# Performance work log

Hardware: AMD Instinct MI355X
Metric: run time of the kernel (lower is better)

The kernel has to match this reference:

```python
import jax, jax.numpy as jnp
import numpy as np

N = 50000      # nodes
E = 600000     # edges (avg degree 12)
IN = 128       # in_feat
HID = IN // 2  # 64
OUT = 128      # out_feat (must equal in_feat, see msg_linear)

# NOTE: the torch source uses nn.LeakyReLU(True): the positional arg is
# negative_slope, so slope == 1.0 (identity). We reproduce that faithfully.
NEG_SLOPE = 1.0

def leaky(v):
    return jnp.where(v >= 0, v, NEG_SLOPE * v)

def _linear_params(key, fan_in, fan_out):
    kw, kb = jax.random.split(key)
    bound = 1.0 / np.sqrt(fan_in)
    W = jax.random.uniform(kw, (fan_in, fan_out), jnp.float32, -bound, bound)
    b = jax.random.uniform(kb, (fan_out,), jnp.float32, -bound, bound)
    return W, b

def setup_inputs() -> dict:
    key = jax.random.key(0)
    ks = jax.random.split(key, 10)
    x = jax.random.normal(ks[0], (N, IN), jnp.float32)
    e = jax.random.normal(ks[1], (E, IN), jnp.float32)
    src = jax.random.randint(ks[2], (E,), 0, N, jnp.int64)
    dst = jax.random.randint(ks[3], (E,), 0, N, jnp.int64)
    W_nl1, b_nl1 = _linear_params(ks[4], IN, HID)    # node_linear1
    W_el, b_el = _linear_params(ks[5], IN, HID)      # edge_linear
    W1, b1 = _linear_params(ks[6], HID, HID)         # node_mlp layer 1
    W2, b2 = _linear_params(ks[7], HID, OUT)         # node_mlp layer 2
    W_nl2, b_nl2 = _linear_params(ks[8], IN, HID)    # node_linear2
    km, ke = jax.random.split(ks[9])
    W_ml, b_ml = _linear_params(km, IN, HID)         # msg_linear (in_feat==out_feat)
    W_em, b_em = _linear_params(ke, HID, OUT)        # edge_mlp layer
    return dict(x=x, e=e, src=src, dst=dst,
                W_nl1=W_nl1, b_nl1=b_nl1, W_el=W_el, b_el=b_el,
                W1=W1, b1=b1, W2=W2, b2=b2,
                W_nl2=W_nl2, b_nl2=b_nl2, W_ml=W_ml, b_ml=b_ml,
                W_em=W_em, b_em=b_em)

def reference(x, e, src, dst,
              W_nl1, b_nl1, W_el, b_el,
              W1, b1, W2, b2,
              W_nl2, b_nl2, W_ml, b_ml,
              W_em, b_em):
    # apply_edges: e' = node_mlp(node_linear1(x[src]) + edge_linear(e))
    z = x[src] @ W_nl1 + b_nl1 + e @ W_el + b_el            # [E, HID]
    e_new = leaky(leaky(z) @ W1 + b1) @ W2 + b2             # [E, OUT]
    # update_all(copy_e, sum): scatter-sum edge messages to destination nodes
    msg = jax.ops.segment_sum(e_new, dst, num_segments=N)   # [N, OUT]
    # x' = edge_mlp(node_linear2(x) + msg_linear(msg))
    h = leaky(x @ W_nl2 + b_nl2 + msg @ W_ml + b_ml)        # [N, HID]
    return h @ W_em + b_em                                  # [N, OUT]
```

## Files before the change

kernel.cpp:

```cpp
#include <hip/hip_runtime.h>

#define N_NODES 50000
#define N_EDGES 600000

typedef float v2f __attribute__((ext_vector_type(2)));

#define WF_PX   0
#define WF_ES   3200000
#define WF_PXS  9600000
#define WF_UN   12800000
#define WI_CNT   16000000
#define WI_OFF   16050000
#define WI_CUR   16100000
#define WI_BSUM  16150000
#define WI_BOFF  16150256
#define WI_EPAIR 16150512
#define WF_T2   17350528
#define WF_BEG  17354624
#define WF_RH   17354752
#define WF_K1   17354816
#define WF_WA   17358912
#define WF_WX1  17375296
#define WF_R    17383488
#define WF_C2   17383616

#define NBLK_SCAN 196

__global__ __launch_bounds__(256) void pre_t2_kernel(
        const float* __restrict__ W2, const float* __restrict__ W_ml,
        const float* __restrict__ b1, const float* __restrict__ b2,
        float* __restrict__ T2, float* __restrict__ be_g) {
    int idx = blockIdx.x * 256 + threadIdx.x;
    if (idx < 4096) {
        int i = idx >> 6, j = idx & 63;
        float s = 0.f;
        for (int k = 0; k < 128; ++k) s += W2[i*128+k] * W_ml[k*64+j];
        T2[idx] = s;
    } else if (idx < 4224) {
        int j = idx - 4096;
        float s = b2[j];
        for (int k = 0; k < 64; ++k) s += b1[k] * W2[k*128+j];
        be_g[j] = s;
    }
}

__global__ __launch_bounds__(256) void pre_k1_kernel(
        const float* __restrict__ W1, const float* __restrict__ T2,
        float* __restrict__ K1) {
    int idx = blockIdx.x * 256 + threadIdx.x;
    if (idx >= 4096) return;
    int i = idx >> 6, j = idx & 63;
    float s = 0.f;
    for (int k = 0; k < 64; ++k) s += W1[i*64+k] * T2[k*64+j];
    K1[idx] = s;
}

__global__ __launch_bounds__(256) void pre_wa_kernel(
        const float* __restrict__ W_nl1, const float* __restrict__ W_el,
        const float* __restrict__ W_nl2, const float* __restrict__ K1,
        const float* __restrict__ b_nl1, const float* __restrict__ b_el,
        const float* __restrict__ be_g, const float* __restrict__ W_ml,
        float* __restrict__ WA, float* __restrict__ WX1,
        float* __restrict__ rh_g) {
    int idx = blockIdx.x * 256 + threadIdx.x;
    if (idx < 8192) {
        WA[idx] = W_nl2[idx];
    } else if (idx < 16384) {
        int p = idx - 8192; int i = p >> 6, j = p & 63;
        float s = 0.f;
        for (int k = 0; k < 64; ++k) s += W_el[i*64+k] * K1[k*64+j];
        WA[idx] = s;
    } else if (idx < 24576) {
        int p = idx - 16384; int i = p >> 6, j = p & 63;
        float s = 0.f;
        for (int k = 0; k < 64; ++k) s += W_nl1[i*64+k] * K1[k*64+j];
        WX1[p] = s;
    } else if (idx < 24640) {
        int t = idx - 24576;
        float s = 0.f;
        for (int k = 0; k < 64; ++k)  s += (b_nl1[k] + b_el[k]) * K1[k*64+t];
        for (int k = 0; k < 128; ++k) s += be_g[k] * W_ml[k*64+t];
        rh_g[t] = s;
    }
}

__global__ __launch_bounds__(256) void pre_rc_kernel(
        const float* __restrict__ rh_g, const float* __restrict__ W_em,
        const float* __restrict__ b_nl2, const float* __restrict__ b_ml,
        const float* __restrict__ b_em,
        float* __restrict__ r, float* __restrict__ c2) {
    int idx = threadIdx.x;
    if (idx < 128) {
        float s = 0.f;
        for (int k = 0; k < 64; ++k) s += rh_g[k] * W_em[k*128+idx];
        r[idx] = s;
    } else {
        int j = idx - 128;
        float s = b_em[j];
        for (int k = 0; k < 64; ++k) s += (b_nl2[k] + b_ml[k]) * W_em[k*128+j];
        c2[j] = s;
    }
}

__global__ __launch_bounds__(256) void zero_kernel(int* __restrict__ cnt) {
    int i = blockIdx.x * 256 + threadIdx.x;
    if (i < N_NODES) cnt[i] = 0;
}

__global__ __launch_bounds__(256) void hist_kernel(const int* __restrict__ dst,
                                                   int* __restrict__ cnt) {
    int e = blockIdx.x * 256 + threadIdx.x;
    if (e < N_EDGES) atomicAdd(&cnt[dst[e]], 1);
}

__global__ __launch_bounds__(256) void scan_a_kernel(const int* __restrict__ cnt,
                                                     int* __restrict__ bsum) {
    __shared__ int s[256];
    int i = blockIdx.x * 256 + threadIdx.x;
    int v = (i < N_NODES) ? cnt[i] : 0;
    s[threadIdx.x] = v;
    __syncthreads();
    for (int d = 128; d > 0; d >>= 1) {
        if (threadIdx.x < d) s[threadIdx.x] += s[threadIdx.x + d];
        __syncthreads();
    }
    if (threadIdx.x == 0) bsum[blockIdx.x] = s[0];
}

__global__ __launch_bounds__(256) void scan_b_kernel(const int* __restrict__ bsum,
                                                     int* __restrict__ boff) {
    __shared__ int s[256];
    int t = threadIdx.x;
    int v = (t < NBLK_SCAN) ? bsum[t] : 0;
    s[t] = v;
    __syncthreads();
    for (int d = 1; d < 256; d <<= 1) {
        int tv = (t >= d) ? s[t - d] : 0;
        __syncthreads();
        s[t] += tv;
        __syncthreads();
    }
    if (t < NBLK_SCAN) boff[t] = s[t] - v;
}

__global__ __launch_bounds__(256) void scan_c_kernel(const int* __restrict__ cnt,
                                                     const int* __restrict__ boff,
                                                     int* __restrict__ offs,
                                                     int* __restrict__ cursor) {
    __shared__ int s[256];
    int i = blockIdx.x * 256 + threadIdx.x;
    int t = threadIdx.x;
    int v = (i < N_NODES) ? cnt[i] : 0;
    s[t] = v;
    __syncthreads();
    for (int d = 1; d < 256; d <<= 1) {
        int tv = (t >= d) ? s[t - d] : 0;
        __syncthreads();
        s[t] += tv;
        __syncthreads();
    }
    if (i < N_NODES) {
        int ex = s[t] - v + boff[blockIdx.x];
        offs[i] = ex;
        cursor[i] = ex;
    }
}

__global__ __launch_bounds__(256) void fill_kernel(const int* __restrict__ dst,
                                                   const int* __restrict__ src,
                                                   int* __restrict__ cursor,
                                                   int2* __restrict__ epair) {
    int e = blockIdx.x * 256 + threadIdx.x;
    if (e < N_EDGES) {
        int pos = atomicAdd(&cursor[dst[e]], 1);
        epair[pos] = make_int2(e, src[e]);
    }
}

__global__ __launch_bounds__(256) void px_kernel(
        const float* __restrict__ x, const float* __restrict__ WX1,
        float* __restrict__ px) {
    __shared__ float As[32][133];
    __shared__ float Ws[32][64];
    int base = blockIdx.x * 128;
    int t = threadIdx.x;
    int cg = t & 15, rg = t >> 4;
    int c0 = cg * 4, r0 = rg * 8;

    float acc[8][4];
    #pragma unroll
    for (int i = 0; i < 8; ++i)
        #pragma unroll
        for (int j = 0; j < 4; ++j) acc[i][j] = 0.f;

    int arow0 = t >> 3;
    int akq   = t & 7;

    for (int k0 = 0; k0 < 128; k0 += 32) {
        __syncthreads();
        #pragma unroll
        for (int i = 0; i < 4; ++i) {
            int row = arow0 + i * 32;
            int n = base + row;
            float4 v = make_float4(0.f, 0.f, 0.f, 0.f);
            if (n < N_NODES)
                v = *(const float4*)&x[(size_t)n * 128 + k0 + akq * 4];
            As[akq * 4 + 0][row] = v.x;
            As[akq * 4 + 1][row] = v.y;
            As[akq * 4 + 2][row] = v.z;
            As[akq * 4 + 3][row] = v.w;
        }
        #pragma unroll
        for (int i = 0; i < 2; ++i) {
            int idx = t + i * 256;
            int row = idx >> 4, q4 = idx & 15;
            *(float4*)&Ws[row][q4 * 4] =
                *(const float4*)&WX1[(size_t)(k0 + row) * 64 + q4 * 4];
        }
        __syncthreads();
        #pragma unroll 8
        for (int k = 0; k < 32; ++k) {
            float a[8];
            *(float4*)&a[0] = *(const float4*)&As[k][r0];
            *(float4*)&a[4] = *(const float4*)&As[k][r0 + 4];
            float4 w = *(const float4*)&Ws[k][c0];
            #pragma unroll
            for (int i = 0; i < 8; ++i) {
                acc[i][0] += a[i] * w.x;
                acc[i][1] += a[i] * w.y;
                acc[i][2] += a[i] * w.z;
                acc[i][3] += a[i] * w.w;
            }
        }
    }

    #pragma unroll
    for (int i = 0; i < 8; ++i) {
        int n = base + r0 + i;
        if (n < N_NODES)
            *(float4*)&px[(size_t)n * 64 + c0] = *(float4*)&acc[i][0];
    }
}

__global__ __launch_bounds__(256) void gather_kernel(
        const float* __restrict__ px, const float* __restrict__ ef,
        const int* __restrict__ cnt, const int* __restrict__ offs,
        const int2* __restrict__ epair,
        float* __restrict__ pxs, float* __restrict__ es) {
    int n    = (int)((blockIdx.x * 256 + threadIdx.x) >> 6);
    int lane = threadIdx.x & 63;
    if (n >= N_NODES) return;
    int off = offs[n], deg = cnt[n];
    int col2 = lane * 2;
    float apx = 0.f, ae0 = 0.f, ae1 = 0.f;
    for (int c0 = 0; c0 < deg; c0 += 64) {
        int j = c0 + lane;
        int2 p = make_int2(0, 0);
        if (j < deg) p = epair[off + j];
        int m = deg - c0; if (m > 64) m = 64;
        for (int j2 = 0; j2 < m; j2 += 8) {
            float xv[8]; v2f ev[8]; float msk[8];
            #pragma unroll
            for (int u = 0; u < 8; ++u) {
                int jj = j2 + u;
                int idx = (jj < m) ? jj : (m - 1);
                msk[u] = (jj < m) ? 1.f : 0.f;
                int e_ = __shfl(p.x, idx);
                int s_ = __shfl(p.y, idx);
                xv[u] = px[(size_t)s_ * 64 + lane];
                ev[u] = __builtin_nontemporal_load(
                            (const v2f*)(ef + (size_t)e_ * 128 + col2));
            }
            #pragma unroll
            for (int u = 0; u < 8; ++u) {
                apx += msk[u] * xv[u];
                ae0 += msk[u] * ev[u][0];
                ae1 += msk[u] * ev[u][1];
            }
        }
    }
    pxs[(size_t)n * 64 + lane] = apx;
    *(float2*)(es + (size_t)n * 128 + col2) = make_float2(ae0, ae1);
}

__global__ __launch_bounds__(256) void gemm1_kernel(
        const float* __restrict__ x, const float* __restrict__ es,
        const float* __restrict__ pxs, const float* __restrict__ WA,
        float* __restrict__ u) {
    __shared__ float As[32][133];
    __shared__ float Ws[32][64];
    int base = blockIdx.x * 128;
    int t = threadIdx.x;
    int cg = t & 15, rg = t >> 4;
    int c0 = cg * 4, r0 = rg * 8;

    float acc[8][4];
    #pragma unroll
    for (int i = 0; i < 8; ++i) {
        int n = base + r0 + i;
        float4 pv = make_float4(0.f, 0.f, 0.f, 0.f);
        if (n < N_NODES) pv = *(const float4*)&pxs[(size_t)n * 64 + c0];
        acc[i][0] = pv.x; acc[i][1] = pv.y; acc[i][2] = pv.z; acc[i][3] = pv.w;
    }

    int arow0 = t >> 3;
    int akq   = t & 7;

    #pragma unroll
    for (int m = 0; m < 2; ++m) {
        const float* __restrict__ S = (m == 0) ? x : es;
        for (int k0 = 0; k0 < 128; k0 += 32) {
            __syncthreads();
            #pragma unroll
            for (int i = 0; i < 4; ++i) {
                int row = arow0 + i * 32;
                int n = base + row;
                float4 v = make_float4(0.f, 0.f, 0.f, 0.f);
                if (n < N_NODES)
                    v = *(const float4*)&S[(size_t)n * 128 + k0 + akq * 4];
                As[akq * 4 + 0][row] = v.x;
                As[akq * 4 + 1][row] = v.y;
                As[akq * 4 + 2][row] = v.z;
                As[akq * 4 + 3][row] = v.w;
            }
            #pragma unroll
            for (int i = 0; i < 2; ++i) {
                int idx = t + i * 256;
                int row = idx >> 4, q4 = idx & 15;
                *(float4*)&Ws[row][q4 * 4] =
                    *(const float4*)&WA[(size_t)(m * 128 + k0 + row) * 64 + q4 * 4];
            }
            __syncthreads();
            #pragma unroll 8
            for (int k = 0; k < 32; ++k) {
                float a[8];
                *(float4*)&a[0] = *(const float4*)&As[k][r0];
                *(float4*)&a[4] = *(const float4*)&As[k][r0 + 4];
                float4 w = *(const float4*)&Ws[k][c0];
                #pragma unroll
                for (int i = 0; i < 8; ++i) {
                    acc[i][0] += a[i] * w.x;
                    acc[i][1] += a[i] * w.y;
                    acc[i][2] += a[i] * w.z;
                    acc[i][3] += a[i] * w.w;
                }
            }
        }
    }

    #pragma unroll
    for (int i = 0; i < 8; ++i) {
        int n = base + r0 + i;
        if (n < N_NODES)
            *(float4*)&u[(size_t)n * 64 + c0] = *(float4*)&acc[i][0];
    }
}

__global__ __launch_bounds__(256) void gemm2_kernel(
        const float* __restrict__ u, const int* __restrict__ cnt,
        const float* __restrict__ W_em,
        const float* __restrict__ rvec, const float* __restrict__ c2,
        float* __restrict__ out) {
    __shared__ float UsT[64][69];
    __shared__ float Wem[64][128];
    int base = blockIdx.x * 64;
    int t = threadIdx.x;
    int cg = t & 15, rg = t >> 4;
    int c0 = cg * 8, r0 = rg * 4;

    #pragma unroll
    for (int i = 0; i < 4; ++i) {
        int idx = t + i * 256;
        int row = idx >> 4, kq = idx & 15;
        int n = base + row;
        float4 v = make_float4(0.f, 0.f, 0.f, 0.f);
        if (n < N_NODES) v = *(const float4*)&u[(size_t)n * 64 + kq * 4];
        UsT[kq * 4 + 0][row] = v.x;
        UsT[kq * 4 + 1][row] = v.y;
        UsT[kq * 4 + 2][row] = v.z;
        UsT[kq * 4 + 3][row] = v.w;
    }
    #pragma unroll
    for (int i = 0; i < 8; ++i) {
        int idx = t + i * 256;
        int row = idx >> 5, q4 = idx & 31;
        *(float4*)&Wem[row][q4 * 4] = *(const float4*)&W_em[(size_t)row * 128 + q4 * 4];
    }

    float4 rva = *(const float4*)&rvec[c0];
    float4 rvb = *(const float4*)&rvec[c0 + 4];
    float4 cva = *(const float4*)&c2[c0];
    float4 cvb = *(const float4*)&c2[c0 + 4];
    float acc[4][8];
    #pragma unroll
    for (int i = 0; i < 4; ++i) {
        int n = base + r0 + i;
        float dg = (n < N_NODES) ? (float)cnt[n] : 0.f;
        acc[i][0] = cva.x + dg * rva.x;  acc[i][1] = cva.y + dg * rva.y;
        acc[i][2] = cva.z + dg * rva.z;  acc[i][3] = cva.w + dg * rva.w;
        acc[i][4] = cvb.x + dg * rvb.x;  acc[i][5] = cvb.y + dg * rvb.y;
        acc[i][6] = cvb.z + dg * rvb.z;  acc[i][7] = cvb.w + dg * rvb.w;
    }
    __syncthreads();

    #pragma unroll 8
    for (int k = 0; k < 64; ++k) {
        float a[4], w[8];
        *(float4*)&a[0] = *(const float4*)&UsT[k][r0];
        *(float4*)&w[0] = *(const float4*)&Wem[k][c0];
        *(float4*)&w[4] = *(const float4*)&Wem[k][c0 + 4];
        #pragma unroll
        for (int i = 0; i < 4; ++i)
            #pragma unroll
            for (int j = 0; j < 8; ++j)
                acc[i][j] += a[i] * w[j];
    }

    #pragma unroll
    for (int i = 0; i < 4; ++i) {
        int n = base + r0 + i;
        if (n < N_NODES) {
            *(float4*)&out[(size_t)n * 128 + c0]     = *(float4*)&acc[i][0];
            *(float4*)&out[(size_t)n * 128 + c0 + 4] = *(float4*)&acc[i][4];
        }
    }
}

extern "C" void kernel_launch(void* const* d_in, const int* in_sizes, int n_in,
                              void* d_out, int out_size, void* d_ws, size_t ws_size,
                              hipStream_t stream) {
    const float* x     = (const float*)d_in[0];
    const float* ef    = (const float*)d_in[1];
    const int*   src   = (const int*)d_in[2];
    const int*   dst   = (const int*)d_in[3];
    const float* W_nl1 = (const float*)d_in[4];
    const float* b_nl1 = (const float*)d_in[5];
    const float* W_el  = (const float*)d_in[6];
    const float* b_el  = (const float*)d_in[7];
    const float* W1    = (const float*)d_in[8];
    const float* b1    = (const float*)d_in[9];
    const float* W2    = (const float*)d_in[10];
    const float* b2    = (const float*)d_in[11];
    const float* W_nl2 = (const float*)d_in[12];
    const float* b_nl2 = (const float*)d_in[13];
    const float* W_ml  = (const float*)d_in[14];
    const float* b_ml  = (const float*)d_in[15];
    const float* W_em  = (const float*)d_in[16];
    const float* b_em  = (const float*)d_in[17];

    int*   wsI = (int*)d_ws;
    float* wsF = (float*)d_ws;
    float* px     = wsF + WF_PX;
    float* es     = wsF + WF_ES;
    float* pxs    = wsF + WF_PXS;
    float* uN     = wsF + WF_UN;
    int*   cnt    = wsI + WI_CNT;
    int*   offs   = wsI + WI_OFF;
    int*   cursor = wsI + WI_CUR;
    int*   bsum   = wsI + WI_BSUM;
    int*   boff   = wsI + WI_BOFF;
    int2*  epair  = (int2*)(wsI + WI_EPAIR);
    float* T2   = wsF + WF_T2;
    float* be_g = wsF + WF_BEG;
    float* rh_g = wsF + WF_RH;
    float* K1   = wsF + WF_K1;
    float* WA   = wsF + WF_WA;
    float* WX1  = wsF + WF_WX1;
    float* r    = wsF + WF_R;
    float* c2   = wsF + WF_C2;

    pre_t2_kernel<<<17, 256, 0, stream>>>(W2, W_ml, b1, b2, T2, be_g);
    pre_k1_kernel<<<16, 256, 0, stream>>>(W1, T2, K1);
    pre_wa_kernel<<<97, 256, 0, stream>>>(W_nl1, W_el, W_nl2, K1,
                                          b_nl1, b_el, be_g, W_ml, WA, WX1, rh_g);
    pre_rc_kernel<<<1, 256, 0, stream>>>(rh_g, W_em, b_nl2, b_ml, b_em, r, c2);

    zero_kernel<<<NBLK_SCAN, 256, 0, stream>>>(cnt);
    hist_kernel<<<(N_EDGES + 255) / 256, 256, 0, stream>>>(dst, cnt);
    scan_a_kernel<<<NBLK_SCAN, 256, 0, stream>>>(cnt, bsum);
    scan_b_kernel<<<1, 256, 0, stream>>>(bsum, boff);
    scan_c_kernel<<<NBLK_SCAN, 256, 0, stream>>>(cnt, boff, offs, cursor);
    fill_kernel<<<(N_EDGES + 255) / 256, 256, 0, stream>>>(dst, src, cursor, epair);

    px_kernel<<<(N_NODES + 127) / 128, 256, 0, stream>>>(x, WX1, px);

    gather_kernel<<<(N_NODES + 3) / 4, 256, 0, stream>>>(
        px, ef, cnt, offs, epair, pxs, es);

    gemm1_kernel<<<(N_NODES + 127) / 128, 256, 0, stream>>>(x, es, pxs, WA, uN);
    gemm2_kernel<<<(N_NODES + 63) / 64, 256, 0, stream>>>(
        uN, cnt, W_em, r, c2, (float*)d_out);
}
```

Before: 252.2 us.

## Project edge features before aggregation and scatter projected rows into CSR order

The per-edge features are no longer gathered at full 128 width and projected after aggregation. A new proj_kernel streams e once, in order, multiplies it by the 128x64 edge weight, and writes each 64-wide result to its CSR slot. The node projections for x (the W_nl2 part and the W_nl1·K1 part) are fused into one 128-wide GEMM. The gather then sums narrow 64-wide rows, contiguous for edges and random for sources, straight into u, and the separate gemm1 pass is removed. The cost is a 600k×64 intermediate written with a scattered row store, plus an extra pos array.

```diff
diff --git a/kernel.cpp b/kernel.cpp
--- a/kernel.cpp
+++ b/kernel.cpp
@@ -4,25 +4,26 @@
 #define N_EDGES 600000
 
 typedef float v2f __attribute__((ext_vector_type(2)));
-
-#define WF_PX   0
-#define WF_ES   3200000
-#define WF_PXS  9600000
-#define WF_UN   12800000
-#define WI_CNT   16000000
-#define WI_OFF   16050000
-#define WI_CUR   16100000
-#define WI_BSUM  16150000
-#define WI_BOFF  16150256
-#define WI_EPAIR 16150512
-#define WF_T2   17350528
-#define WF_BEG  17354624
-#define WF_RH   17354752
-#define WF_K1   17354816
-#define WF_WA   17358912
-#define WF_WX1  17375296
-#define WF_R    17383488
-#define WF_C2   17383616
+typedef float v4f __attribute__((ext_vector_type(4)));
+
+#define WF_PA    0
+#define WF_EFP   6400000
+#define WF_UN    44800000
+#define WI_CNT   48000000
+#define WI_OFF   48050000
+#define WI_CUR   48100000
+#define WI_BSUM  48150000
+#define WI_BOFF  48150256
+#define WI_POS   48150512
+#define WI_ESRC  48750512
+#define WF_T2    49350528
+#define WF_BEG   49354624
+#define WF_RH    49354752
+#define WF_K1    49354816
+#define WF_WAX   49358912
+#define WF_WE    49375296
+#define WF_R     49383488
+#define WF_C2    49383616
 
 #define NBLK_SCAN 196
 
@@ -60,21 +61,23 @@
         const float* __restrict__ W_nl2, const float* __restrict__ K1,
         const float* __restrict__ b_nl1, const float* __restrict__ b_el,
         const float* __restrict__ be_g, const float* __restrict__ W_ml,
-        float* __restrict__ WA, float* __restrict__ WX1,
+        float* __restrict__ WAX, float* __restrict__ WE,
         float* __restrict__ rh_g) {
     int idx = blockIdx.x * 256 + threadIdx.x;
-    if (idx < 8192) {
-        WA[idx] = W_nl2[idx];
-    } else if (idx < 16384) {
-        int p = idx - 8192; int i = p >> 6, j = p & 63;
-        float s = 0.f;
-        for (int k = 0; k < 64; ++k) s += W_el[i*64+k] * K1[k*64+j];
-        WA[idx] = s;
+    if (idx < 16384) {
+        int i = idx >> 7, j = idx & 127;
+        if (j < 64) {
+            WAX[idx] = W_nl2[i*64+j];
+        } else {
+            float s = 0.f;
+            for (int k = 0; k < 64; ++k) s += W_nl1[i*64+k] * K1[k*64+(j-64)];
+            WAX[idx] = s;
+        }
     } else if (idx < 24576) {
         int p = idx - 16384; int i = p >> 6, j = p & 63;
         float s = 0.f;
-        for (int k = 0; k < 64; ++k) s += W_nl1[i*64+k] * K1[k*64+j];
-        WX1[p] = s;
+        for (int k = 0; k < 64; ++k) s += W_el[i*64+k] * K1[k*64+j];
+        WE[p] = s;
     } else if (idx < 24640) {
         int t = idx - 24576;
         float s = 0.f;
@@ -166,32 +169,34 @@
     }
 }
 
-__global__ __launch_bounds__(256) void fill_kernel(const int* __restrict__ dst,
-                                                   const int* __restrict__ src,
-                                                   int* __restrict__ cursor,
-                                                   int2* __restrict__ epair) {
+__global__ __launch_bounds__(256) void fill2_kernel(const int* __restrict__ dst,
+                                                    const int* __restrict__ src,
+                                                    int* __restrict__ cursor,
+                                                    int* __restrict__ pos,
+                                                    int* __restrict__ esrc) {
     int e = blockIdx.x * 256 + threadIdx.x;
     if (e < N_EDGES) {
-        int pos = atomicAdd(&cursor[dst[e]], 1);
-        epair[pos] = make_int2(e, src[e]);
-    }
-}
-
-__global__ __launch_bounds__(256) void px_kernel(
-        const float* __restrict__ x, const float* __restrict__ WX1,
-        float* __restrict__ px) {
+        int p = atomicAdd(&cursor[dst[e]], 1);
+        pos[e] = p;
+        esrc[p] = src[e];
+    }
+}
+
+__global__ __launch_bounds__(256) void pa_kernel(
+        const float* __restrict__ x, const float* __restrict__ WAX,
+        float* __restrict__ PA) {
     __shared__ float As[32][133];
-    __shared__ float Ws[32][64];
+    __shared__ float Ws[32][128];
     int base = blockIdx.x * 128;
     int t = threadIdx.x;
     int cg = t & 15, rg = t >> 4;
-    int c0 = cg * 4, r0 = rg * 8;
-
-    float acc[8][4];
+    int c0 = cg * 8, r0 = rg * 8;
+
+    float acc[8][8];
     #pragma unroll
     for (int i = 0; i < 8; ++i)
         #pragma unroll
-        for (int j = 0; j < 4; ++j) acc[i][j] = 0.f;
+        for (int j = 0; j < 8; ++j) acc[i][j] = 0.f;
 
     int arow0 = t >> 3;
     int akq   = t & 7;
@@ -211,11 +216,78 @@
             As[akq * 4 + 3][row] = v.w;
         }
         #pragma unroll
+        for (int i = 0; i < 4; ++i) {
+            int idx = t + i * 256;
+            int row = idx >> 5, q4 = idx & 31;
+            *(float4*)&Ws[row][q4 * 4] =
+                *(const float4*)&WAX[(size_t)(k0 + row) * 128 + q4 * 4];
+        }
+        __syncthreads();
+        #pragma unroll 8
+        for (int k = 0; k < 32; ++k) {
+            float a[8], w[8];
+            *(float4*)&a[0] = *(const float4*)&As[k][r0];
+            *(float4*)&a[4] = *(const float4*)&As[k][r0 + 4];
+            *(float4*)&w[0] = *(const float4*)&Ws[k][c0];
+            *(float4*)&w[4] = *(const float4*)&Ws[k][c0 + 4];
+            #pragma unroll
+            for (int i = 0; i < 8; ++i)
+                #pragma unroll
+                for (int jj = 0; jj < 8; ++jj)
+                    acc[i][jj] += a[i] * w[jj];
+        }
+    }
+
+    #pragma unroll
+    for (int i = 0; i < 8; ++i) {
+        int n = base + r0 + i;
+        if (n < N_NODES) {
+            *(float4*)&PA[(size_t)n * 128 + c0]     = *(float4*)&acc[i][0];
+            *(float4*)&PA[(size_t)n * 128 + c0 + 4] = *(float4*)&acc[i][4];
+        }
+    }
+}
+
+__global__ __launch_bounds__(256) void proj_kernel(
+        const float* __restrict__ ef, const float* __restrict__ WE,
+        const int* __restrict__ pos, float* __restrict__ efp) {
+    __shared__ float As[32][133];
+    __shared__ float Ws[32][64];
+    int base = blockIdx.x * 128;
+    int t = threadIdx.x;
+    int cg = t & 15, rg = t >> 4;
+    int c0 = cg * 4, r0 = rg * 8;
+
+    float acc[8][4];
+    #pragma unroll
+    for (int i = 0; i < 8; ++i)
+        #pragma unroll
+        for (int j = 0; j < 4; ++j) acc[i][j] = 0.f;
+
+    int arow0 = t >> 3;
+    int akq   = t & 7;
+
+    for (int k0 = 0; k0 < 128; k0 += 32) {
+        __syncthreads();
+        #pragma unroll
+        for (int i = 0; i < 4; ++i) {
+            int row = arow0 + i * 32;
+            int e = base + row;
+            v4f v = {0.f, 0.f, 0.f, 0.f};
+            if (e < N_EDGES)
+                v = __builtin_nontemporal_load(
+                        (const v4f*)&ef[(size_t)e * 128 + k0 + akq * 4]);
+            As[akq * 4 + 0][row] = v[0];
+            As[akq * 4 + 1][row] = v[1];
+            As[akq * 4 + 2][row] = v[2];
+            As[akq * 4 + 3][row] = v[3];
+        }
+        #pragma unroll
         for (int i = 0; i < 2; ++i) {
             int idx = t + i * 256;
             int row = idx >> 4, q4 = idx & 15;
             *(float4*)&Ws[row][q4 * 4] =
-                *(const float4*)&WX1[(size_t)(k0 + row) * 64 + q4 * 4];
+                *(const float4*)&WE[(size_t)(k0 + row) * 64 + q4 * 4];
         }
         __syncthreads();
         #pragma unroll 8
@@ -236,124 +308,49 @@
 
     #pragma unroll
     for (int i = 0; i < 8; ++i) {
-        int n = base + r0 + i;
-        if (n < N_NODES)
-            *(float4*)&px[(size_t)n * 64 + c0] = *(float4*)&acc[i][0];
-    }
-}
-
-__global__ __launch_bounds__(256) void gather_kernel(
-        const float* __restrict__ px, const float* __restrict__ ef,
+        int e = base + r0 + i;
+        if (e < N_EDGES)
+            *(float4*)&efp[(size_t)pos[e] * 64 + c0] = *(float4*)&acc[i][0];
+    }
+}
+
+__global__ __launch_bounds__(256) void gather2_kernel(
+        const float* __restrict__ PA, const float* __restrict__ efp,
         const int* __restrict__ cnt, const int* __restrict__ offs,
-        const int2* __restrict__ epair,
-        float* __restrict__ pxs, float* __restrict__ es) {
-    int n    = (int)((blockIdx.x * 256 + threadIdx.x) >> 6);
-    int lane = threadIdx.x & 63;
+        const int* __restrict__ esrc, float* __restrict__ u) {
+    int wid  = (int)((blockIdx.x * 256 + threadIdx.x) >> 6);
+    int half = (threadIdx.x >> 5) & 1;
+    int hl   = threadIdx.x & 31;
+    int n    = wid * 2 + half;
     if (n >= N_NODES) return;
     int off = offs[n], deg = cnt[n];
-    int col2 = lane * 2;
-    float apx = 0.f, ae0 = 0.f, ae1 = 0.f;
-    for (int c0 = 0; c0 < deg; c0 += 64) {
-        int j = c0 + lane;
-        int2 p = make_int2(0, 0);
-        if (j < deg) p = epair[off + j];
-        int m = deg - c0; if (m > 64) m = 64;
+    int col2 = hl * 2;
+    float2 av = *(const float2*)&PA[(size_t)n * 128 + col2];
+    float au0 = av.x, au1 = av.y;
+    for (int c0 = 0; c0 < deg; c0 += 32) {
+        int j = c0 + hl;
+        int myS = (j < deg) ? esrc[off + j] : 0;
+        int m = deg - c0; if (m > 32) m = 32;
         for (int j2 = 0; j2 < m; j2 += 8) {
-            float xv[8]; v2f ev[8]; float msk[8];
+            v2f pv[8], ev[8]; float msk[8];
             #pragma unroll
-            for (int u = 0; u < 8; ++u) {
-                int jj = j2 + u;
+            for (int uu = 0; uu < 8; ++uu) {
+                int jj = j2 + uu;
                 int idx = (jj < m) ? jj : (m - 1);
-                msk[u] = (jj < m) ? 1.f : 0.f;
-                int e_ = __shfl(p.x, idx);
-                int s_ = __shfl(p.y, idx);
-                xv[u] = px[(size_t)s_ * 64 + lane];
-                ev[u] = __builtin_nontemporal_load(
-                            (const v2f*)(ef + (size_t)e_ * 128 + col2));
+                msk[uu] = (jj < m) ? 1.f : 0.f;
+                int s_ = __shfl(myS, (half << 5) | idx);
+                int row = off + c0 + idx;
+                ev[uu] = *(const v2f*)(efp + (size_t)row * 64 + col2);
+                pv[uu] = *(const v2f*)(PA + (size_t)s_ * 128 + 64 + col2);
             }
             #pragma unroll
-            for (int u = 0; u < 8; ++u) {
-                apx += msk[u] * xv[u];
-                ae0 += msk[u] * ev[u][0];
-                ae1 += msk[u] * ev[u][1];
+            for (int uu = 0; uu < 8; ++uu) {
+                au0 += msk[uu] * (ev[uu][0] + pv[uu][0]);
+                au1 += msk[uu] * (ev[uu][1] + pv[uu][1]);
             }
         }
     }
-    pxs[(size_t)n * 64 + lane] = apx;
-    *(float2*)(es + (size_t)n * 128 + col2) = make_float2(ae0, ae1);
-}
-
-__global__ __launch_bounds__(256) void gemm1_kernel(
-        const float* __restrict__ x, const float* __restrict__ es,
-        const float* __restrict__ pxs, const float* __restrict__ WA,
-        float* __restrict__ u) {
-    __shared__ float As[32][133];
-    __shared__ float Ws[32][64];
-    int base = blockIdx.x * 128;
-    int t = threadIdx.x;
-    int cg = t & 15, rg = t >> 4;
-    int c0 = cg * 4, r0 = rg * 8;
-
-    float acc[8][4];
-    #pragma unroll
-    for (int i = 0; i < 8; ++i) {
-        int n = base + r0 + i;
-        float4 pv = make_float4(0.f, 0.f, 0.f, 0.f);
-        if (n < N_NODES) pv = *(const float4*)&pxs[(size_t)n * 64 + c0];
-        acc[i][0] = pv.x; acc[i][1] = pv.y; acc[i][2] = pv.z; acc[i][3] = pv.w;
-    }
-
-    int arow0 = t >> 3;
-    int akq   = t & 7;
-
-    #pragma unroll
-    for (int m = 0; m < 2; ++m) {
-        const float* __restrict__ S = (m == 0) ? x : es;
-        for (int k0 = 0; k0 < 128; k0 += 32) {
-            __syncthreads();
-            #pragma unroll
-            for (int i = 0; i < 4; ++i) {
-                int row = arow0 + i * 32;
-                int n = base + row;
-                float4 v = make_float4(0.f, 0.f, 0.f, 0.f);
-                if (n < N_NODES)
-                    v = *(const float4*)&S[(size_t)n * 128 + k0 + akq * 4];
-                As[akq * 4 + 0][row] = v.x;
-                As[akq * 4 + 1][row] = v.y;
-                As[akq * 4 + 2][row] = v.z;
-                As[akq * 4 + 3][row] = v.w;
-            }
-            #pragma unroll
-            for (int i = 0; i < 2; ++i) {
-                int idx = t + i * 256;
-                int row = idx >> 4, q4 = idx & 15;
-                *(float4*)&Ws[row][q4 * 4] =
-                    *(const float4*)&WA[(size_t)(m * 128 + k0 + row) * 64 + q4 * 4];
-            }
-            __syncthreads();
-            #pragma unroll 8
-            for (int k = 0; k < 32; ++k) {
-                float a[8];
-                *(float4*)&a[0] = *(const float4*)&As[k][r0];
-                *(float4*)&a[4] = *(const float4*)&As[k][r0 + 4];
-                float4 w = *(const float4*)&Ws[k][c0];
-                #pragma unroll
-                for (int i = 0; i < 8; ++i) {
-                    acc[i][0] += a[i] * w.x;
-                    acc[i][1] += a[i] * w.y;
-                    acc[i][2] += a[i] * w.z;
-                    acc[i][3] += a[i] * w.w;
-                }
-            }
-        }
-    }
-
-    #pragma unroll
-    for (int i = 0; i < 8; ++i) {
-        int n = base + r0 + i;
-        if (n < N_NODES)
-            *(float4*)&u[(size_t)n * 64 + c0] = *(float4*)&acc[i][0];
-    }
+    *(float2*)&u[(size_t)n * 64 + col2] = make_float2(au0, au1);
 }
 
 __global__ __launch_bounds__(256) void gemm2_kernel(
@@ -450,44 +447,45 @@
 
     int*   wsI = (int*)d_ws;
     float* wsF = (float*)d_ws;
-    float* px     = wsF + WF_PX;
-    float* es     = wsF + WF_ES;
-    float* pxs    = wsF + WF_PXS;
+    float* PA     = wsF + WF_PA;
+    float* efp    = wsF + WF_EFP;
     float* uN     = wsF + WF_UN;
     int*   cnt    = wsI + WI_CNT;
     int*   offs   = wsI + WI_OFF;
     int*   cursor = wsI + WI_CUR;
     int*   bsum   = wsI + WI_BSUM;
     int*   boff   = wsI + WI_BOFF;
-    int2*  epair  = (int2*)(wsI + WI_EPAIR);
+    int*   pos    = wsI + WI_POS;
+    int*   esrc   = wsI + WI_ESRC;
     float* T2   = wsF + WF_T2;
     float* be_g = wsF + WF_BEG;
     float* rh_g = wsF + WF_RH;
     float* K1   = wsF + WF_K1;
-    float* WA   = wsF + WF_WA;
-    float* WX1  = wsF + WF_WX1;
+    float* WAX  = wsF + WF_WAX;
+    float* WE   = wsF + WF_WE;
     float* r    = wsF + WF_R;
     float* c2   = wsF + WF_C2;
 
     pre_t2_kernel<<<17, 256, 0, stream>>>(W2, W_ml, b1, b2, T2, be_g);
+    zero_kernel<<<NBLK_SCAN, 256, 0, stream>>>(cnt);
     pre_k1_kernel<<<16, 256, 0, stream>>>(W1, T2, K1);
+    hist_kernel<<<(N_EDGES + 255) / 256, 256, 0, stream>>>(dst, cnt);
     pre_wa_kernel<<<97, 256, 0, stream>>>(W_nl1, W_el, W_nl2, K1,
-                                          b_nl1, b_el, be_g, W_ml, WA, WX1, rh_g);
-    pre_rc_kernel<<<1, 256, 0, stream>>>(rh_g, W_em, b_nl2, b_ml, b_em, r, c2);
-
-    zero_kernel<<<NBLK_SCAN, 256, 0, stream>>>(cnt);
-    hist_kernel<<<(N_EDGES + 255) / 256, 256, 0, stream>>>(dst, cnt);
+                                          b_nl1, b_el, be_g, W_ml, WAX, WE, rh_g);
     scan_a_kernel<<<NBLK_SCAN, 256, 0, stream>>>(cnt, bsum);
     scan_b_kernel<<<1, 256, 0, stream>>>(bsum, boff);
     scan_c_kernel<<<NBLK_SCAN, 256, 0, stream>>>(cnt, boff, offs, cursor);
-    fill_kernel<<<(N_EDGES + 255) / 256, 256, 0, stream>>>(dst, src, cursor, epair);
-
-    px_kernel<<<(N_NODES + 127) / 128, 256, 0, stream>>>(x, WX1, px);
-
-    gather_kernel<<<(N_NODES + 3) / 4, 256, 0, stream>>>(
-        px, ef, cnt, offs, epair, pxs, es);
-
-    gemm1_kernel<<<(N_NODES + 127) / 128, 256, 0, stream>>>(x, es, pxs, WA, uN);
+    pre_rc_kernel<<<1, 256, 0, stream>>>(rh_g, W_em, b_nl2, b_ml, b_em, r, c2);
+    fill2_kernel<<<(N_EDGES + 255) / 256, 256, 0, stream>>>(dst, src, cursor,
+                                                            pos, esrc);
+
+    pa_kernel<<<(N_NODES + 127) / 128, 256, 0, stream>>>(x, WAX, PA);
+
+    proj_kernel<<<(N_EDGES + 127) / 128, 256, 0, stream>>>(ef, WE, pos, efp);
+
+    gather2_kernel<<<(N_NODES + 7) / 8, 256, 0, stream>>>(
+        PA, efp, cnt, offs, esrc, uN);
+
     gemm2_kernel<<<(N_NODES + 63) / 64, 256, 0, stream>>>(
         uN, cnt, W_em, r, c2, (float*)d_out);
 }
```

Result: slower. 350.1 us (+38.8%).
